# Performance work log

Hardware: AMD Instinct MI355X
Metric: run time of the kernel (lower is better)

## Reference

```python
import jax, jax.numpy as jnp
import numpy as np

HIDDEN = 1024
NUM_HEADS = 16
HEAD_DIM = HIDDEN // NUM_HEADS


def setup_inputs() -> dict:
    key = jax.random.key(0)
    ks = jax.random.split(key, 13)
    B, S, H = 4, 2048, HIDDEN
    sc = 1.0 / np.sqrt(H)
    inp = {
        'queries': jax.random.normal(ks[0], (B, S, H), jnp.float32),
        'keys': jax.random.normal(ks[1], (B, S, H), jnp.float32),
        'values': jax.random.normal(ks[2], (B, S, H), jnp.float32),
        'attention_mask': jax.random.randint(ks[3], (B, S, S), 0, 2, jnp.int32),
        'W_q': jax.random.normal(ks[4], (H, H), jnp.float32) * sc,
        'b_q': jnp.zeros((H,), jnp.float32),
        'W_k': jax.random.normal(ks[5], (H, H), jnp.float32) * sc,
        'b_k': jnp.zeros((H,), jnp.float32),
        'W_v': jax.random.normal(ks[6], (H, H), jnp.float32) * sc,
        'b_v': jnp.zeros((H,), jnp.float32),
        'W_o': jax.random.normal(ks[7], (H, H), jnp.float32) * sc,
        'b_o': jnp.zeros((H,), jnp.float32),
    }
    return inp


def _split_heads(x):
    # [B, S, H] -> [B, nH, S, d]
    B, S, _ = x.shape
    return x.reshape(B, S, NUM_HEADS, HEAD_DIM).transpose(0, 2, 1, 3)


def reference(queries, keys, values, attention_mask, W_q, b_q, W_k, b_k, W_v, b_v, W_o, b_o):
    q = _split_heads(queries @ W_q + b_q)   # [B, nH, S, d]
    k = _split_heads(keys @ W_k + b_k)
    v = _split_heads(values @ W_v + b_v)
    d = q.shape[-1]
    scores = jnp.einsum('bhqd,bhkd->bhqk', q, k) / jnp.sqrt(jnp.float32(d))
    # mask repeat_interleave over heads == broadcast mask over head axis
    mask = attention_mask[:, None, :, :]    # [B, 1, S, S]
    scores = jnp.where(mask == 0, jnp.float32(-1e6), scores)
    attn = jax.nn.softmax(scores, axis=-1)  # dropout p=0 -> identity
    out = jnp.einsum('bhqk,bhkd->bhqd', attn, v)  # [B, nH, S, d]
    B, _, S, _ = out.shape
    out = out.transpose(0, 2, 1, 3).reshape(B, S, NUM_HEADS * HEAD_DIM)
    return out @ W_o + b_o
```

## Files before the change

kernel.cpp:

```cpp
#include <hip/hip_runtime.h>
#include <stdint.h>

typedef unsigned short u16;
typedef uint32_t u32;
typedef unsigned long long u64;
typedef short bf16x8 __attribute__((ext_vector_type(8)));
typedef float f32x4 __attribute__((ext_vector_type(4)));
typedef float f32x16 __attribute__((ext_vector_type(16)));

#define MFMA16 __builtin_amdgcn_mfma_f32_16x16x32_bf16
#define MFMA32 __builtin_amdgcn_mfma_f32_32x32x16_bf16
#define L2E 1.44269504088896340736f

static __device__ __forceinline__ u16 f2bf(float f) {
  union { float f; u32 u; } v; v.f = f;
  u32 r = v.u + 0x7FFFu + ((v.u >> 16) & 1u);
  return (u16)(r >> 16);
}

static __device__ __forceinline__ u32 cvtpk(float lo, float hi) {
  u32 r;
  asm("v_cvt_pk_bf16_f32 %0, %1, %2" : "=v"(r) : "v"(lo), "v"(hi));
  return r;
}

static __device__ __forceinline__ void glds16(const u16* g, u16* l) {
  __builtin_amdgcn_global_load_lds((const __attribute__((address_space(1))) void*)g,
                                   (__attribute__((address_space(3))) void*)l, 16, 0, 0);
}

__global__ __launch_bounds__(256) void cvt3_kernel(
    const float* __restrict__ s0, const float* __restrict__ s1, const float* __restrict__ s2,
    u16* __restrict__ d0, u16* __restrict__ d1, u16* __restrict__ d2) {
  const float* s = (blockIdx.z == 0) ? s0 : (blockIdx.z == 1) ? s1 : s2;
  u16* d = (blockIdx.z == 0) ? d0 : (blockIdx.z == 1) ? d1 : d2;
  size_t i = ((size_t)blockIdx.x * 256 + threadIdx.x) * 8;
  float4 a = *(const float4*)(s + i);
  float4 c = *(const float4*)(s + i + 4);
  bf16x8 o;
  o[0] = (short)f2bf(a.x); o[1] = (short)f2bf(a.y);
  o[2] = (short)f2bf(a.z); o[3] = (short)f2bf(a.w);
  o[4] = (short)f2bf(c.x); o[5] = (short)f2bf(c.y);
  o[6] = (short)f2bf(c.z); o[7] = (short)f2bf(c.w);
  *(bf16x8*)(d + i) = o;
}

__global__ __launch_bounds__(256) void wtrans_kernel(
    const float* __restrict__ w0, const float* __restrict__ w1,
    const float* __restrict__ w2, const float* __restrict__ w3,
    u16* __restrict__ t0, u16* __restrict__ t1, u16* __restrict__ t2, u16* __restrict__ t3) {
  const float* w = (blockIdx.z == 0) ? w0 : (blockIdx.z == 1) ? w1 : (blockIdx.z == 2) ? w2 : w3;
  u16* t = (blockIdx.z == 0) ? t0 : (blockIdx.z == 1) ? t1 : (blockIdx.z == 2) ? t2 : t3;
  __shared__ float tile[64][65];
  const int bx = blockIdx.x, by = blockIdx.y;
#pragma unroll
  for (int i = 0; i < 16; ++i) {
    int idx = i * 256 + threadIdx.x;
    int r = idx >> 6, c = idx & 63;
    tile[r][c] = w[(size_t)(by * 64 + r) * 1024 + bx * 64 + c];
  }
  __syncthreads();
#pragma unroll
  for (int i = 0; i < 16; ++i) {
    int idx = i * 256 + threadIdx.x;
    int r = idx >> 6, c = idx & 63;
    t[(size_t)(bx * 64 + r) * 1024 + by * 64 + c] = f2bf(tile[c][r]);
  }
}

__global__ __launch_bounds__(256) void packmask_kernel(const int* __restrict__ m,
                                                       u32* __restrict__ pmo) {
  const size_t i = (size_t)blockIdx.x * 256 + threadIdx.x;
  const int lane = threadIdx.x & 63;
  unsigned long long b = __ballot(m[i] != 0);
  if (lane == 0) pmo[i >> 5] = (u32)b;
  else if (lane == 32) pmo[i >> 5] = (u32)(b >> 32);
}

template <int OM>
__global__ __launch_bounds__(512, 2) void gemm_kernel(
    const u16* __restrict__ A, const u16* __restrict__ Bt, const float* __restrict__ bias,
    void* __restrict__ Cout, float oscale) {
  constexpr int K = 1024, N = 1024;
  constexpr int NT = K / 64;
  __shared__ u16 As[3][256 * 64];
  __shared__ u16 Bs[3][128 * 64];
  const int tid = threadIdx.x;
  const int lane = tid & 63;
  const int wid = tid >> 6;
  const int l15 = lane & 15;
  const int lg = lane >> 4;
  const int orig = blockIdx.x;
  const int wgid = (orig & 7) * 32 + (orig >> 3);
  const int row0 = (wgid >> 3) * 256;
  const int col0 = (wgid & 7) * 128;
  const int wr = wid >> 1, wc = wid & 1;
  const int swf = (l15 & 7) << 3;
  const f32x4 fzero = {0.f, 0.f, 0.f, 0.f};

  f32x4 acc[4][4];
#pragma unroll
  for (int m = 0; m < 4; ++m)
#pragma unroll
    for (int n = 0; n < 4; ++n) acc[m][n] = fzero;

#define GSTAGE(buf, k0)                                                        \
  do {                                                                         \
    _Pragma("unroll") for (int i = 0; i < 4; ++i) {                            \
      int e = (i * 512 + tid) * 8;                                             \
      int r = e >> 6, c = e & 63;                                              \
      int cs = c ^ ((r & 7) << 3);                                             \
      glds16(A + (size_t)(row0 + r) * K + (k0) + cs, &As[buf][e]);             \
    }                                                                          \
    _Pragma("unroll") for (int i = 0; i < 2; ++i) {                            \
      int e = (i * 512 + tid) * 8;                                             \
      int r = e >> 6, c = e & 63;                                              \
      int cs = c ^ ((r & 7) << 3);                                             \
      glds16(Bt + (size_t)(col0 + r) * K + (k0) + cs, &Bs[buf][e]);            \
    }                                                                          \
  } while (0)

  GSTAGE(0, 0);
  GSTAGE(1, 64);
  asm volatile("s_waitcnt vmcnt(6)" ::: "memory");
  __builtin_amdgcn_s_barrier();
  __builtin_amdgcn_sched_barrier(0);

  for (int t = 0; t < NT; ++t) {
    const int buf = t % 3;
    if (t + 2 < NT) GSTAGE((t + 2) % 3, (t + 2) * 64);
    __builtin_amdgcn_sched_barrier(0);

    __builtin_amdgcn_s_setprio(1);
#pragma unroll
    for (int ks = 0; ks < 2; ++ks) {
      const int koff = ks * 32 + lg * 8;
      bf16x8 af[4], bfr[4];
#pragma unroll
      for (int m = 0; m < 4; ++m)
        af[m] = *(const bf16x8*)(&As[buf][(wr * 64 + m * 16 + l15) * 64 + (koff ^ swf)]);
#pragma unroll
      for (int n = 0; n < 4; ++n)
        bfr[n] = *(const bf16x8*)(&Bs[buf][(wc * 64 + n * 16 + l15) * 64 + (koff ^ swf)]);
#pragma unroll
      for (int m = 0; m < 4; ++m)
#pragma unroll
        for (int n = 0; n < 4; ++n)
          acc[m][n] = MFMA16(af[m], bfr[n], acc[m][n], 0, 0, 0);
    }
    __builtin_amdgcn_s_setprio(0);

    if (t + 1 < NT) {
      if (t + 2 < NT)
        asm volatile("s_waitcnt vmcnt(6)" ::: "memory");
      else
        asm volatile("s_waitcnt vmcnt(0)" ::: "memory");
      __builtin_amdgcn_s_barrier();
      __builtin_amdgcn_sched_barrier(0);
    }
  }
#undef GSTAGE

#pragma unroll
  for (int n = 0; n < 4; ++n) {
    const int col = col0 + wc * 64 + n * 16 + l15;
    const float bv = bias[col];
#pragma unroll
    for (int m = 0; m < 4; ++m) {
#pragma unroll
      for (int r = 0; r < 4; ++r) {
        const int row = row0 + wr * 64 + m * 16 + lg * 4 + r;
        const float v = (acc[m][n][r] + bv) * oscale;
        if constexpr (OM == 0) {
          ((u16*)Cout)[(size_t)row * N + col] = f2bf(v);
        } else if constexpr (OM == 1) {
          ((float*)Cout)[(size_t)row * N + col] = v;
        } else {
          const int b_ = row >> 11, s_ = row & 2047, h_ = col >> 6, d_ = col & 63;
          ((u16*)Cout)[(size_t)((b_ * 16 + h_) * 64 + d_) * 2048 + s_] = f2bf(v);
        }
      }
    }
  }
}

__global__ __launch_bounds__(256, 4) void attn_kernel(
    const u16* __restrict__ Qb, const u16* __restrict__ Kb, const u16* __restrict__ Vt,
    const u32* __restrict__ pm, u16* __restrict__ Oa) {
  __shared__ u16 Ks[2][64 * 64];
  __shared__ u16 Vs[2][64 * 64];
  __shared__ uint4 mlut[16];
  const int tid = threadIdx.x;
  const int lane = tid & 63;
  const int wid = tid >> 6;
  const int c31 = lane & 31;
  const int hi = lane >> 5;
  const int orig = blockIdx.x;
  const int wgid = (orig & 7) * 128 + (orig >> 3);
  const int qt = wgid & 15;
  const int hh = (wgid >> 4) & 15;
  const int bb = wgid >> 8;
  const int qbase = qt * 128 + wid * 32;
  const int sw = (lane & 7) << 3;

  if (tid < 16)
    mlut[tid] = make_uint4((u32) - (int)(tid & 1), (u32) - (int)((tid >> 1) & 1),
                           (u32) - (int)((tid >> 2) & 1), (u32) - (int)((tid >> 3) & 1));

  const size_t qrow = (size_t)(bb * 2048 + qbase + c31);
  bf16x8 qf[4];
#pragma unroll
  for (int ds = 0; ds < 4; ++ds)
    qf[ds] = *(const bf16x8*)(Qb + qrow * 1024 + hh * 64 + ds * 16 + hi * 8);

  float lrun = 0.f;
  f32x16 oacc[2];
#pragma unroll
  for (int dn = 0; dn < 2; ++dn)
#pragma unroll
    for (int r = 0; r < 16; ++r) oacc[dn][r] = 0.f;

  const size_t kgbase = (size_t)(bb * 2048) * 1024 + hh * 64;
  const size_t vgbase = (size_t)((bb * 16 + hh) * 64) * 2048;

#define STAGE(buf, kbase)                                                              \
  do {                                                                                 \
    _Pragma("unroll") for (int i = 0; i < 2; ++i) {                                    \
      int r = ((i * 256 + tid) * 8) >> 6, c = ((i * 256 + tid) * 8) & 63;              \
      int cs = c ^ ((r & 7) << 3);                                                     \
      glds16(Kb + kgbase + (size_t)((kbase) + r) * 1024 + cs,                          \
             &Ks[buf][(i * 256 + wid * 64) * 8]);                                      \
      glds16(Vt + vgbase + (size_t)r * 2048 + (kbase) + cs,                            \
             &Vs[buf][(i * 256 + wid * 64) * 8]);                                      \
    }                                                                                  \
  } while (0)

  STAGE(0, 0);
  __syncthreads();

  int cur = 0;
  for (int kt = 0; kt < 32; ++kt) {
    if (kt < 31) STAGE(cur ^ 1, (kt + 1) * 64);

    const u64 mw = *(const u64*)(pm + qrow * 64 + kt * 2);
    float ps = 0.f;

#pragma unroll
    for (int kb = 0; kb < 2; ++kb) {
      f32x16 sacc;
#pragma unroll
      for (int r = 0; r < 16; ++r) sacc[r] = 0.f;
#pragma unroll
      for (int ds = 0; ds < 4; ++ds) {
        bf16x8 kf = *(const bf16x8*)(&Ks[cur][(kb * 32 + c31) * 64 + ((ds * 16 + hi * 8) ^ sw)]);
        sacc = MFMA32(kf, qf[ds], sacc, 0, 0, 0);
      }

      const u32 mwk = (u32)(mw >> (kb * 32));
      u32 Ap[4], Bp[4];
#pragma unroll
      for (int q2 = 0; q2 < 4; ++q2) {
        const u32 kb4 = (mwk >> (q2 * 8 + hi * 4)) & 0xFu;
        const uint4 mm = mlut[kb4];
        const float p0 = __builtin_amdgcn_exp2f(sacc[4 * q2 + 0]);
        const float p1 = __builtin_amdgcn_exp2f(sacc[4 * q2 + 1]);
        const float p2 = __builtin_amdgcn_exp2f(sacc[4 * q2 + 2]);
        const float p3 = __builtin_amdgcn_exp2f(sacc[4 * q2 + 3]);
        const float f0 = __uint_as_float(__float_as_uint(p0) & mm.x);
        const float f1 = __uint_as_float(__float_as_uint(p1) & mm.y);
        const float f2 = __uint_as_float(__float_as_uint(p2) & mm.z);
        const float f3 = __uint_as_float(__float_as_uint(p3) & mm.w);
        ps += (f0 + f1) + (f2 + f3);
        Ap[q2] = cvtpk(f0, f1);
        Bp[q2] = cvtpk(f2, f3);
      }

      asm("v_permlane32_swap_b32 %0, %1" : "+v"(Ap[0]), "+v"(Ap[1]));
      asm("v_permlane32_swap_b32 %0, %1" : "+v"(Bp[0]), "+v"(Bp[1]));
      asm("v_permlane32_swap_b32 %0, %1" : "+v"(Ap[2]), "+v"(Ap[3]));
      asm("v_permlane32_swap_b32 %0, %1" : "+v"(Bp[2]), "+v"(Bp[3]));

#pragma unroll
      for (int t = 0; t < 2; ++t) {
        uint4 fr;
        fr.x = Ap[2 * t]; fr.y = Bp[2 * t]; fr.z = Ap[2 * t + 1]; fr.w = Bp[2 * t + 1];
        const bf16x8 pf = *(const bf16x8*)&fr;
        const int koff = (kb * 2 + t) * 16 + hi * 8;
#pragma unroll
        for (int dn = 0; dn < 2; ++dn) {
          bf16x8 vf = *(const bf16x8*)(&Vs[cur][(dn * 32 + c31) * 64 + (koff ^ sw)]);
          oacc[dn] = MFMA32(vf, pf, oacc[dn], 0, 0, 0);
        }
      }
    }

    ps += __shfl_xor(ps, 32);
    lrun += ps;

    __syncthreads();
    cur ^= 1;
  }
#undef STAGE

  const float inv = 1.0f / lrun;
  u16* orow = Oa + qrow * 1024 + hh * 64;
#pragma unroll
  for (int dn = 0; dn < 2; ++dn) {
#pragma unroll
    for (int q2 = 0; q2 < 4; ++q2) {
      uint2 w;
      w.x = cvtpk(oacc[dn][4 * q2 + 0] * inv, oacc[dn][4 * q2 + 1] * inv);
      w.y = cvtpk(oacc[dn][4 * q2 + 2] * inv, oacc[dn][4 * q2 + 3] * inv);
      *(uint2*)(orow + dn * 32 + q2 * 8 + hi * 4) = w;
    }
  }
}

extern "C" void kernel_launch(void* const* d_in, const int* in_sizes, int n_in,
                              void* d_out, int out_size, void* d_ws, size_t ws_size,
                              hipStream_t stream) {
  const float* q = (const float*)d_in[0];
  const float* k = (const float*)d_in[1];
  const float* v = (const float*)d_in[2];
  const int* mask = (const int*)d_in[3];
  const float* Wq = (const float*)d_in[4]; const float* bq = (const float*)d_in[5];
  const float* Wk = (const float*)d_in[6]; const float* bk = (const float*)d_in[7];
  const float* Wv = (const float*)d_in[8]; const float* bv = (const float*)d_in[9];
  const float* Wo = (const float*)d_in[10]; const float* bo = (const float*)d_in[11];
  float* out = (float*)d_out;
  char* ws = (char*)d_ws;
  const size_t MB = 1024ull * 1024ull;
  u16* qbf = (u16*)(ws + 0 * MB);
  u16* kbf = (u16*)(ws + 16 * MB);
  u16* vbf = (u16*)(ws + 32 * MB);
  u16* Qp  = (u16*)(ws + 48 * MB);
  u16* Kp  = (u16*)(ws + 64 * MB);
  u16* Vtp = (u16*)(ws + 80 * MB);
  u16* Wqt = (u16*)(ws + 96 * MB);
  u16* Wkt = (u16*)(ws + 98 * MB);
  u16* Wvt = (u16*)(ws + 100 * MB);
  u16* Wot = (u16*)(ws + 102 * MB);
  u32* pmb = (u32*)(ws + 104 * MB);
  u16* Oa  = qbf;

  const float QSCALE = 0.125f * L2E;

  cvt3_kernel<<<dim3(4096, 1, 3), 256, 0, stream>>>(q, k, v, qbf, kbf, vbf);
  wtrans_kernel<<<dim3(16, 16, 4), 256, 0, stream>>>(Wq, Wk, Wv, Wo, Wqt, Wkt, Wvt, Wot);
  packmask_kernel<<<dim3(65536), 256, 0, stream>>>(mask, pmb);
  gemm_kernel<0><<<dim3(256), 512, 0, stream>>>(qbf, Wqt, bq, Qp, QSCALE);
  gemm_kernel<0><<<dim3(256), 512, 0, stream>>>(kbf, Wkt, bk, Kp, 1.0f);
  gemm_kernel<2><<<dim3(256), 512, 0, stream>>>(vbf, Wvt, bv, Vtp, 1.0f);
  attn_kernel<<<dim3(1024), 256, 0, stream>>>(Qp, Kp, Vtp, pmb, Oa);
  gemm_kernel<1><<<dim3(256), 512, 0, stream>>>(Oa, Wot, bo, out, 1.0f);
}
```

Before: 263.8 us.

## Interleave global-to-LDS staging with LDS reads and MFMA phases in GEMM loop

Splits the per-iteration global-to-LDS prefetch into two halves. Each half is issued between the LDS fragment reads and the MFMA block of one k-substep, with barriers and lgkmcnt waits placed in a ping-pong style schedule. The aim is to spread memory-issue pressure across the iteration and overlap it with matrix math. It adds two extra workgroup barriers per iteration, which may cost more than the overlap gains.

```diff
diff --git a/kernel.cpp b/kernel.cpp
--- a/kernel.cpp
+++ b/kernel.cpp
@@ -104,15 +104,15 @@
 #pragma unroll
     for (int n = 0; n < 4; ++n) acc[m][n] = fzero;
 
-#define GSTAGE(buf, k0)                                                        \
+#define GSTAGE_PART(buf, k0, a0, a1, b0, b1)                                   \
   do {                                                                         \
-    _Pragma("unroll") for (int i = 0; i < 4; ++i) {                            \
+    _Pragma("unroll") for (int i = (a0); i < (a1); ++i) {                      \
       int e = (i * 512 + tid) * 8;                                             \
       int r = e >> 6, c = e & 63;                                              \
       int cs = c ^ ((r & 7) << 3);                                             \
       glds16(A + (size_t)(row0 + r) * K + (k0) + cs, &As[buf][e]);             \
     }                                                                          \
-    _Pragma("unroll") for (int i = 0; i < 2; ++i) {                            \
+    _Pragma("unroll") for (int i = (b0); i < (b1); ++i) {                      \
       int e = (i * 512 + tid) * 8;                                             \
       int r = e >> 6, c = e & 63;                                              \
       int cs = c ^ ((r & 7) << 3);                                             \
@@ -120,21 +120,20 @@
     }                                                                          \
   } while (0)
 
-  GSTAGE(0, 0);
-  GSTAGE(1, 64);
+  GSTAGE_PART(0, 0, 0, 4, 0, 2);
+  GSTAGE_PART(1, 64, 0, 4, 0, 2);
   asm volatile("s_waitcnt vmcnt(6)" ::: "memory");
   __builtin_amdgcn_s_barrier();
   __builtin_amdgcn_sched_barrier(0);
 
   for (int t = 0; t < NT; ++t) {
     const int buf = t % 3;
-    if (t + 2 < NT) GSTAGE((t + 2) % 3, (t + 2) * 64);
-    __builtin_amdgcn_sched_barrier(0);
-
-    __builtin_amdgcn_s_setprio(1);
-#pragma unroll
-    for (int ks = 0; ks < 2; ++ks) {
-      const int koff = ks * 32 + lg * 8;
+    const int buf2 = (t + 2) % 3;
+    const int k2 = (t + 2) * 64;
+    const bool stg = (t + 2 < NT);
+
+    {
+      const int koff = 0 * 32 + lg * 8;
       bf16x8 af[4], bfr[4];
 #pragma unroll
       for (int m = 0; m < 4; ++m)
@@ -142,13 +141,44 @@
 #pragma unroll
       for (int n = 0; n < 4; ++n)
         bfr[n] = *(const bf16x8*)(&Bs[buf][(wc * 64 + n * 16 + l15) * 64 + (koff ^ swf)]);
+      if (stg) GSTAGE_PART(buf2, k2, 0, 2, 0, 1);
+      __builtin_amdgcn_sched_barrier(0);
+      __builtin_amdgcn_s_barrier();
+      asm volatile("s_waitcnt lgkmcnt(0)" ::: "memory");
+      __builtin_amdgcn_sched_barrier(0);
+      __builtin_amdgcn_s_setprio(1);
 #pragma unroll
       for (int m = 0; m < 4; ++m)
 #pragma unroll
         for (int n = 0; n < 4; ++n)
           acc[m][n] = MFMA16(af[m], bfr[n], acc[m][n], 0, 0, 0);
-    }
-    __builtin_amdgcn_s_setprio(0);
+      __builtin_amdgcn_s_setprio(0);
+      __builtin_amdgcn_sched_barrier(0);
+      __builtin_amdgcn_s_barrier();
+    }
+
+    {
+      const int koff = 1 * 32 + lg * 8;
+      bf16x8 af[4], bfr[4];
+#pragma unroll
+      for (int m = 0; m < 4; ++m)
+        af[m] = *(const bf16x8*)(&As[buf][(wr * 64 + m * 16 + l15) * 64 + (koff ^ swf)]);
+#pragma unroll
+      for (int n = 0; n < 4; ++n)
+        bfr[n] = *(const bf16x8*)(&Bs[buf][(wc * 64 + n * 16 + l15) * 64 + (koff ^ swf)]);
+      if (stg) GSTAGE_PART(buf2, k2, 2, 4, 1, 2);
+      __builtin_amdgcn_sched_barrier(0);
+      __builtin_amdgcn_s_barrier();
+      asm volatile("s_waitcnt lgkmcnt(0)" ::: "memory");
+      __builtin_amdgcn_sched_barrier(0);
+      __builtin_amdgcn_s_setprio(1);
+#pragma unroll
+      for (int m = 0; m < 4; ++m)
+#pragma unroll
+        for (int n = 0; n < 4; ++n)
+          acc[m][n] = MFMA16(af[m], bfr[n], acc[m][n], 0, 0, 0);
+      __builtin_amdgcn_s_setprio(0);
+    }
 
     if (t + 1 < NT) {
       if (t + 2 < NT)
@@ -159,7 +189,7 @@
       __builtin_amdgcn_sched_barrier(0);
     }
   }
-#undef GSTAGE
+#undef GSTAGE_PART
 
 #pragma unroll
   for (int n = 0; n < 4; ++n) {
```

Result: faster. 245.9 us (-6.8%).
